# Kernel tuning notes

Measured on AMD Instinct MI355X. Metric: run time of the kernel, lower is better.

The kernel has to match this reference:

```python
import jax, jax.numpy as jnp
import numpy as np

B, T, W, L, H, TW = 2, 4096, 2048, 2048, 8, 4
HD = L // H  # head dim for block-diagonal gate projections


def setup_inputs() -> dict:
    key = jax.random.key(0)
    ks = jax.random.split(key, 16)
    inv_sqrt_w = 1.0 / np.sqrt(W)
    inv_sqrt_l = 1.0 / np.sqrt(L)
    inv_sqrt_hd = 1.0 / np.sqrt(HD)
    return {
        "x": jax.random.normal(ks[0], (B, T, W), dtype=jnp.float32),
        "segment_pos": jnp.tile(jnp.arange(T, dtype=jnp.int32), (B, 1)),
        # linear_y, linear_x: width -> lru_width
        "w_y": jax.random.normal(ks[1], (W, L), dtype=jnp.float32) * inv_sqrt_w,
        "b_y": jnp.zeros((L,), dtype=jnp.float32),
        "w_x": jax.random.normal(ks[2], (W, L), dtype=jnp.float32) * inv_sqrt_w,
        "b_x": jnp.zeros((L,), dtype=jnp.float32),
        # linear_out: lru_width -> width
        "w_out": jax.random.normal(ks[3], (L, W), dtype=jnp.float32) * inv_sqrt_l,
        "b_out": jnp.zeros((W,), dtype=jnp.float32),
        # depthwise causal temporal conv, kernel [TW, L]
        "conv_w": jax.random.normal(ks[4], (TW, L), dtype=jnp.float32) / np.sqrt(TW),
        "conv_b": jnp.zeros((L,), dtype=jnp.float32),
        # RG-LRU: a_param and two block-diagonal gate projections
        "a_param": jax.random.uniform(ks[5], (L,), dtype=jnp.float32, minval=-2.0, maxval=1.0),
        "igate_w": jax.random.normal(ks[6], (H, HD, HD), dtype=jnp.float32) * inv_sqrt_hd,
        "igate_b": jnp.zeros((H, HD), dtype=jnp.float32),
        "agate_w": jax.random.normal(ks[7], (H, HD, HD), dtype=jnp.float32) * inv_sqrt_hd,
        "agate_b": jnp.zeros((H, HD), dtype=jnp.float32),
    }


def _block_diag_linear(u, w, b):
    # u: [B,T,L] -> [B,T,H,HD] blockwise projected -> [B,T,L]
    uh = u.reshape(u.shape[0], u.shape[1], H, HD)
    y = jnp.einsum("bthd,hde->bthe", uh, w) + b
    return y.reshape(u.shape)


def _forward(x, segment_pos, w_y, b_y, w_x, b_x, w_out, b_out,
             conv_w, conv_b, a_param, igate_w, igate_b, agate_w, agate_b):
    # gate branch: linear_y + tanh-approx GELU
    y = jax.nn.gelu(jnp.einsum("btw,wl->btl", x, w_y) + b_y, approximate=True)
    # recurrent branch: linear_x
    xb = jnp.einsum("btw,wl->btl", x, w_x) + b_x
    # causal depthwise temporal conv (width TW), zero history before t=0
    x_pad = jnp.pad(xb, ((0, 0), (TW - 1, 0), (0, 0)))
    conv = conv_b + sum(conv_w[j] * x_pad[:, j:j + T] for j in range(TW))
    # RG-LRU gates
    gate_x = jax.nn.sigmoid(_block_diag_linear(conv, igate_w, igate_b))
    gate_a = jax.nn.sigmoid(_block_diag_linear(conv, agate_w, agate_b))
    log_a = -8.0 * gate_a * jax.nn.softplus(a_param)  # [B,T,L]
    a = jnp.exp(log_a)
    reset = (segment_pos == 0)[..., None]  # [B,T,1]
    multiplier = jnp.sqrt(1.0 - jnp.exp(2.0 * log_a))
    multiplier = jnp.where(reset, 1.0, multiplier)
    normed = conv * gate_x * multiplier
    a_masked = jnp.where(reset, 0.0, a)
    # diagonal linear recurrence: h_t = a_t * h_{t-1} + normed_t
    def step(h, inp):
        a_t, x_t = inp
        h = a_t * h + x_t
        return h, h
    h0 = jnp.zeros((x.shape[0], L), dtype=x.dtype)
    _, hs = jax.lax.scan(step, h0, (a_masked.transpose(1, 0, 2), normed.transpose(1, 0, 2)))
    hs = hs.transpose(1, 0, 2)  # [B,T,L]
    # elementwise gate then output projection
    return jnp.einsum("btl,lw->btw", hs * y, w_out) + b_out


def reference(x, segment_pos, w_y, b_y, w_x, b_x, w_out, b_out,
              conv_w, conv_b, a_param, igate_w, igate_b, agate_w, agate_b):
    return _forward(x, segment_pos, w_y, b_y, w_x, b_x, w_out, b_out,
                    conv_w, conv_b, a_param, igate_w, igate_b, agate_w, agate_b)
```

## Files before the change

kernel.cpp:

```cpp
#include <hip/hip_runtime.h>
#include <cstdint>
#include <math.h>

typedef _Float16 f16;
typedef f16 f16x8 __attribute__((ext_vector_type(8)));
typedef f16 f16x4 __attribute__((ext_vector_type(4)));
typedef float f32x4 __attribute__((ext_vector_type(4)));

#define BATCH 2
#define TSEQ 4096
#define WID 2048
#define LRU 2048
#define NHEAD 8
#define HDIM 256
#define MTOT (BATCH * TSEQ)
#define CT 128
#define NC (TSEQ / CT)

__device__ __forceinline__ void gl2lds16(const f16* g, f16* l) {
  __builtin_amdgcn_global_load_lds(
      (__attribute__((address_space(1))) uint32_t*)(uintptr_t)g,
      (__attribute__((address_space(3))) uint32_t*)(uint32_t)(uintptr_t)l,
      16, 0, 0);
}

__device__ __forceinline__ float sigmoidf_(float x) { return 1.f / (1.f + expf(-x)); }
__device__ __forceinline__ float f16bits_to_f(uint32_t b) {
  return (float)__builtin_bit_cast(f16, (uint16_t)b);
}

__global__ void prep_kernel(const float* __restrict__ x, f16* __restrict__ Xh,
                            const float* __restrict__ w_y, const float* __restrict__ w_x,
                            const float* __restrict__ w_out,
                            f16* __restrict__ wyT, f16* __restrict__ wxT, f16* __restrict__ woutT,
                            const float* __restrict__ ig, const float* __restrict__ ag,
                            f16* __restrict__ igT, f16* __restrict__ agT) {
  __shared__ float tile[32][33];
  const int bid = blockIdx.x, t = threadIdx.x;
  if (bid < 16384) {
    int i = bid * 256 + t;
    float4 v = ((const float4*)x)[i];
    f16x4 o = { (f16)v.x, (f16)v.y, (f16)v.z, (f16)v.w };
    ((f16x4*)Xh)[i] = o;
    return;
  }
  const int tx = t & 31, ty = t >> 5;
  const float* ib; f16* ob; int R, C, c0, r0;
  if (bid < 28672) {
    int idx = bid - 16384;
    int z = idx >> 12, tl = idx & 4095;
    ib = z == 0 ? w_y : (z == 1 ? w_x : w_out);
    ob = z == 0 ? wyT : (z == 1 ? wxT : woutT);
    R = 2048; C = 2048;
    c0 = (tl & 63) * 32; r0 = (tl >> 6) * 32;
  } else {
    int idx = bid - 28672;
    int z = idx >> 6, tl = idx & 63;
    ib = (z < 8 ? ig : ag) + (long long)(z & 7) * HDIM * HDIM;
    ob = (z < 8 ? igT : agT) + (long long)(z & 7) * HDIM * HDIM;
    R = HDIM; C = HDIM;
    c0 = (tl & 7) * 32; r0 = (tl >> 3) * 32;
  }
#pragma unroll
  for (int i = 0; i < 32; i += 8)
    tile[ty + i][tx] = ib[(long long)(r0 + ty + i) * C + c0 + tx];
  __syncthreads();
#pragma unroll
  for (int i = 0; i < 32; i += 8)
    ob[(long long)(c0 + ty + i) * R + r0 + tx] = (f16)tile[tx][ty + i];
}

__global__ __launch_bounds__(256, 2) void gemm_dual(
    const f16* __restrict__ A, const f16* __restrict__ B1T, const f16* __restrict__ B2T,
    const float* __restrict__ b1, const float* __restrict__ b2,
    f16* __restrict__ Y, f16* __restrict__ X2, int M, int N, int K) {
  __shared__ __align__(16) f16 As[128 * 32];
  __shared__ __align__(16) f16 B1s[128 * 32];
  __shared__ __align__(16) f16 B2s[128 * 32];
  const int m0 = blockIdx.x * 128, n0 = blockIdx.y * 128;
  const int t = threadIdx.x;
  const int lane = t & 63, wave = t >> 6;
  const int wr = (wave >> 1) * 64, wc = (wave & 1) * 64;
  const int l15 = lane & 15, quad = lane >> 4;
  const int srow = t >> 2, scol = (t & 3) * 8;

  const f16* Ag = A + (long long)(m0 + srow) * K + scol;
  const f16* B1g = B1T + (long long)(n0 + srow) * K + scol;
  const f16* B2g = B2T + (long long)(n0 + srow) * K + scol;

  f32x4 c1[4][4] = {};
  f32x4 c2[4][4] = {};
  for (int k0 = 0; k0 < K; k0 += 32) {
    gl2lds16(Ag, &As[t * 8]);   gl2lds16(Ag + (long long)64 * K, &As[64 * 32 + t * 8]);
    gl2lds16(B1g, &B1s[t * 8]); gl2lds16(B1g + (long long)64 * K, &B1s[64 * 32 + t * 8]);
    gl2lds16(B2g, &B2s[t * 8]); gl2lds16(B2g + (long long)64 * K, &B2s[64 * 32 + t * 8]);
    Ag += 32; B1g += 32; B2g += 32;
    __syncthreads();
    f16x8 af[4], b1f[4], b2f[4];
#pragma unroll
    for (int i = 0; i < 4; ++i)
      af[i] = *(const f16x8*)&As[(wr + i * 16 + l15) * 32 + quad * 8];
#pragma unroll
    for (int j = 0; j < 4; ++j) {
      b1f[j] = *(const f16x8*)&B1s[(wc + j * 16 + l15) * 32 + quad * 8];
      b2f[j] = *(const f16x8*)&B2s[(wc + j * 16 + l15) * 32 + quad * 8];
    }
#pragma unroll
    for (int i = 0; i < 4; ++i)
#pragma unroll
      for (int j = 0; j < 4; ++j) {
        c1[i][j] = __builtin_amdgcn_mfma_f32_16x16x32_f16(af[i], b1f[j], c1[i][j], 0, 0, 0);
        c2[i][j] = __builtin_amdgcn_mfma_f32_16x16x32_f16(af[i], b2f[j], c2[i][j], 0, 0, 0);
      }
    __syncthreads();
  }
#pragma unroll
  for (int i = 0; i < 4; ++i) {
#pragma unroll
    for (int j = 0; j < 4; ++j) {
      const int col = n0 + wc + j * 16 + l15;
      const float b1v = b1[col], b2v = b2[col];
      const int row0 = m0 + wr + i * 16 + quad * 4;
#pragma unroll
      for (int r = 0; r < 4; ++r) {
        long long off = (long long)(row0 + r) * N + col;
        float v = c1[i][j][r] + b1v;
        float u = v + 0.044715f * v * v * v;
        float g = 0.5f * v * (1.f + tanhf(0.7978845608028654f * u));
        Y[off] = (f16)g;
        X2[off] = (f16)(c2[i][j][r] + b2v);
      }
    }
  }
}

__global__ __launch_bounds__(256, 2) void gemm_bt(
    const f16* __restrict__ A, const f16* __restrict__ BT, const float* __restrict__ bias,
    float* __restrict__ Cf, int M, int N, int K) {
  __shared__ __align__(16) f16 As[128 * 32];
  __shared__ __align__(16) f16 Bs[128 * 32];
  const int m0 = blockIdx.x * 128, n0 = blockIdx.y * 128;
  const int t = threadIdx.x;
  const int lane = t & 63, wave = t >> 6;
  const int wr = (wave >> 1) * 64, wc = (wave & 1) * 64;
  const int l15 = lane & 15, quad = lane >> 4;
  const int srow = t >> 2, scol = (t & 3) * 8;

  const f16* Ag = A + (long long)(m0 + srow) * K + scol;
  const f16* Bg = BT + (long long)(n0 + srow) * K + scol;

  f32x4 acc[4][4] = {};
  for (int k0 = 0; k0 < K; k0 += 32) {
    gl2lds16(Ag, &As[t * 8]); gl2lds16(Ag + (long long)64 * K, &As[64 * 32 + t * 8]);
    gl2lds16(Bg, &Bs[t * 8]); gl2lds16(Bg + (long long)64 * K, &Bs[64 * 32 + t * 8]);
    Ag += 32; Bg += 32;
    __syncthreads();
    f16x8 af[4], bf[4];
#pragma unroll
    for (int i = 0; i < 4; ++i)
      af[i] = *(const f16x8*)&As[(wr + i * 16 + l15) * 32 + quad * 8];
#pragma unroll
    for (int j = 0; j < 4; ++j)
      bf[j] = *(const f16x8*)&Bs[(wc + j * 16 + l15) * 32 + quad * 8];
#pragma unroll
    for (int i = 0; i < 4; ++i)
#pragma unroll
      for (int j = 0; j < 4; ++j)
        acc[i][j] = __builtin_amdgcn_mfma_f32_16x16x32_f16(af[i], bf[j], acc[i][j], 0, 0, 0);
    __syncthreads();
  }
#pragma unroll
  for (int i = 0; i < 4; ++i) {
#pragma unroll
    for (int j = 0; j < 4; ++j) {
      const int col = n0 + wc + j * 16 + l15;
      const float bv = bias[col];
      const int row0 = m0 + wr + i * 16 + quad * 4;
#pragma unroll
      for (int r = 0; r < 4; ++r)
        Cf[(long long)(row0 + r) * N + col] = acc[i][j][r] + bv;
    }
  }
}

__global__ __launch_bounds__(256, 2) void gates_fused(
    const f16* __restrict__ XBh, const float* __restrict__ cw, const float* __restrict__ cb,
    const f16* __restrict__ BiT, const f16* __restrict__ BaT,
    const float* __restrict__ ib, const float* __restrict__ ab,
    const float* __restrict__ a_param, const int* __restrict__ segpos,
    uint32_t* __restrict__ AN, float* __restrict__ Ac, float* __restrict__ Hc) {
  __shared__ __align__(16) f16 As[128 * 256];
  __shared__ __align__(16) f16 Bi[128 * 32];
  __shared__ __align__(16) f16 Ba[128 * 32];
  const int m0 = blockIdx.x * 128;
  const int h = blockIdx.y >> 1;
  const int half = blockIdx.y & 1;
  const int ncol0 = h * HDIM + half * 128;
  const int t = threadIdx.x;
  const int lane = t & 63, wave = t >> 6;
  const int wr = (wave >> 1) * 64, wc = (wave & 1) * 64;
  const int l15 = lane & 15, quad = lane >> 4;

#pragma unroll 4
  for (int it = 0; it < 16; ++it) {
    int idx = it * 256 + t;
    int r = idx >> 5, kc = idx & 31;
    int m = m0 + r, tpos = m & (TSEQ - 1);
    int colbase = h * HDIM + kc * 8;
    float acc[8];
    {
      float4 c0 = *(const float4*)&cb[colbase];
      float4 c1 = *(const float4*)&cb[colbase + 4];
      acc[0] = c0.x; acc[1] = c0.y; acc[2] = c0.z; acc[3] = c0.w;
      acc[4] = c1.x; acc[5] = c1.y; acc[6] = c1.z; acc[7] = c1.w;
    }
#pragma unroll
    for (int d = 0; d < 4; ++d) {
      if (tpos >= d) {
        f16x8 xv = *(const f16x8*)&XBh[(long long)(m - d) * LRU + colbase];
        float4 w0 = *(const float4*)&cw[(3 - d) * LRU + colbase];
        float4 w1 = *(const float4*)&cw[(3 - d) * LRU + colbase + 4];
        acc[0] += w0.x * (float)xv[0]; acc[1] += w0.y * (float)xv[1];
        acc[2] += w0.z * (float)xv[2]; acc[3] += w0.w * (float)xv[3];
        acc[4] += w1.x * (float)xv[4]; acc[5] += w1.y * (float)xv[5];
        acc[6] += w1.z * (float)xv[6]; acc[7] += w1.w * (float)xv[7];
      }
    }
    f16x8 o;
#pragma unroll
    for (int k = 0; k < 8; ++k) o[k] = (f16)acc[k];
    int gs = (kc & ~7) | ((kc ^ r) & 7);
    *(f16x8*)&As[r * 256 + gs * 8] = o;
  }
  __syncthreads();

  const int srow = t >> 2, scol = (t & 3) * 8;
  const f16* Big = BiT + (long long)(ncol0 + srow) * HDIM + scol;
  const f16* Bag = BaT + (long long)(ncol0 + srow) * HDIM + scol;
  f32x4 ci[4][4] = {};
  f32x4 ca[4][4] = {};
  for (int k0 = 0; k0 < HDIM; k0 += 32) {
    gl2lds16(Big, &Bi[t * 8]); gl2lds16(Big + 64 * HDIM, &Bi[64 * 32 + t * 8]);
    gl2lds16(Bag, &Ba[t * 8]); gl2lds16(Bag + 64 * HDIM, &Ba[64 * 32 + t * 8]);
    Big += 32; Bag += 32;
    __syncthreads();
    f16x8 af[4], bif[4], baf[4];
#pragma unroll
    for (int i = 0; i < 4; ++i) {
      int row = wr + i * 16 + l15;
      int g = (k0 >> 3) + quad;
      int gsw = (g & ~7) | ((g ^ row) & 7);
      af[i] = *(const f16x8*)&As[row * 256 + gsw * 8];
    }
#pragma unroll
    for (int j = 0; j < 4; ++j) {
      bif[j] = *(const f16x8*)&Bi[(wc + j * 16 + l15) * 32 + quad * 8];
      baf[j] = *(const f16x8*)&Ba[(wc + j * 16 + l15) * 32 + quad * 8];
    }
#pragma unroll
    for (int i = 0; i < 4; ++i)
#pragma unroll
      for (int j = 0; j < 4; ++j) {
        ci[i][j] = __builtin_amdgcn_mfma_f32_16x16x32_f16(af[i], bif[j], ci[i][j], 0, 0, 0);
        ca[i][j] = __builtin_amdgcn_mfma_f32_16x16x32_f16(af[i], baf[j], ca[i][j], 0, 0, 0);
      }
    __syncthreads();
  }

  const int mb = m0 >> 12;
  const int cch = (m0 & (TSEQ - 1)) >> 7;
  float Aw[4], hw[4];
#pragma unroll
  for (int j = 0; j < 4; ++j) {
    const int cl = wc + j * 16 + l15;
    const int col = ncol0 + cl;
    const float ibv = ib[col], abv = ab[col];
    const float sp = log1pf(expf(a_param[col]));
    float A4[4], h4[4];
#pragma unroll
    for (int i = 0; i < 4; ++i) {
      float Aseg = 1.f, hseg = 0.f;
#pragma unroll
      for (int r = 0; r < 4; ++r) {
        const int rowL = wr + i * 16 + quad * 4 + r;
        const int row = m0 + rowL;
        float gx = sigmoidf_(ci[i][j][r] + ibv);
        float ga = sigmoidf_(ca[i][j][r] + abv);
        float la = -8.f * ga * sp;
        bool rs = (segpos[row] == 0);
        float a = rs ? 0.f : expf(la);
        uint32_t afx = __float2uint_rn(a * 65536.f);
        if (afx > 65535u) afx = 65535u;
        float aq = (float)afx * (1.f / 65536.f);
        int cfull = half * 128 + cl;
        int g = cfull >> 3, e = cfull & 7;
        int gsw = (g & ~7) | ((g ^ rowL) & 7);
        float cv = (float)As[rowL * 256 + gsw * 8 + e];
        float mult = rs ? 1.f : sqrtf(fmaxf(1.f - aq * aq, 0.f));
        f16 nh = (f16)(cv * gx * mult);
        AN[(long long)row * LRU + col] =
            afx | ((uint32_t)__builtin_bit_cast(uint16_t, nh) << 16);
        float xq = (float)nh;
        hseg = aq * hseg + xq;
        Aseg *= aq;
      }
      A4[i] = Aseg; h4[i] = hseg;
    }
#pragma unroll
    for (int i = 0; i < 4; ++i) {
      float A = A4[i], hv = h4[i];
#pragma unroll
      for (int d = 1; d <= 2; d <<= 1) {
        int src = quad >= d ? lane - 16 * d : lane;
        float Ap = __shfl(A, src);
        float hp = __shfl(hv, src);
        if (quad >= d) { hv = A * hp + hv; A = Ap * A; }
      }
      A4[i] = __shfl(A, 48 + l15);
      h4[i] = __shfl(hv, 48 + l15);
    }
    float Awv = 1.f, hwv = 0.f;
#pragma unroll
    for (int i = 0; i < 4; ++i) { hwv = A4[i] * hwv + h4[i]; Awv *= A4[i]; }
    Aw[j] = Awv; hw[j] = hwv;
  }
  float* carry = (float*)Bi;
  __syncthreads();
  if (wr == 0 && quad == 0) {
#pragma unroll
    for (int j = 0; j < 4; ++j) {
      int cl = wc + j * 16 + l15;
      carry[cl * 2] = Aw[j]; carry[cl * 2 + 1] = hw[j];
    }
  }
  __syncthreads();
  if (wr == 64 && quad == 0) {
#pragma unroll
    for (int j = 0; j < 4; ++j) {
      int cl = wc + j * 16 + l15;
      float At = carry[cl * 2], ht = carry[cl * 2 + 1];
      float A = At * Aw[j];
      float hv = Aw[j] * ht + hw[j];
      int o = (mb * NC + cch) * LRU + ncol0 + cl;
      Ac[o] = A; Hc[o] = hv;
    }
  }
}

__global__ void scan23_kernel(const uint32_t* __restrict__ AN,
                              const float* __restrict__ Ac, const float* __restrict__ Hc,
                              const f16* __restrict__ Yh, f16* __restrict__ G) {
  int l = blockIdx.x * 256 + threadIdx.x;
  int c = blockIdx.y, b = blockIdx.z;
  float hv = 0.f;
  for (int cc = 0; cc < c; ++cc) {
    int o = (b * NC + cc) * LRU + l;
    hv = Ac[o] * hv + Hc[o];
  }
  long long base = ((long long)b * TSEQ + (long long)c * CT) * LRU + l;
#pragma unroll 4
  for (int s = 0; s < CT; ++s) {
    long long o = base + (long long)s * LRU;
    uint32_t p = AN[o];
    float a = (float)(p & 0xFFFFu) * (1.f / 65536.f);
    float x = f16bits_to_f(p >> 16);
    hv = a * hv + x;
    G[o] = (f16)(hv * (float)Yh[o]);
  }
}

extern "C" void kernel_launch(void* const* d_in, const int* in_sizes, int n_in,
                              void* d_out, int out_size, void* d_ws, size_t ws_size,
                              hipStream_t stream) {
  (void)in_sizes; (void)n_in; (void)out_size; (void)ws_size;
  const float* x          = (const float*)d_in[0];
  const int*   segment_pos= (const int*)d_in[1];
  const float* w_y        = (const float*)d_in[2];
  const float* b_y        = (const float*)d_in[3];
  const float* w_x        = (const float*)d_in[4];
  const float* b_x        = (const float*)d_in[5];
  const float* w_out      = (const float*)d_in[6];
  const float* b_out      = (const float*)d_in[7];
  const float* conv_w     = (const float*)d_in[8];
  const float* conv_b     = (const float*)d_in[9];
  const float* a_param    = (const float*)d_in[10];
  const float* igate_w    = (const float*)d_in[11];
  const float* igate_b    = (const float*)d_in[12];
  const float* agate_w    = (const float*)d_in[13];
  const float* agate_b    = (const float*)d_in[14];
  float* out = (float*)d_out;

  char* base = (char*)d_ws;
  size_t off = 0;
  auto alloc = [&](size_t nbytes) -> void* {
    void* p = base + off;
    off = (off + nbytes + 255) & ~(size_t)255;
    return p;
  };
  f16*     Xh    = (f16*)alloc((size_t)MTOT * LRU * 2);
  f16*     Yh    = (f16*)alloc((size_t)MTOT * LRU * 2);
  f16*     XBh   = (f16*)alloc((size_t)MTOT * LRU * 2);
  uint32_t* AN   = (uint32_t*)alloc((size_t)MTOT * LRU * 4);
  f16*     wyT   = (f16*)alloc((size_t)WID * LRU * 2);
  f16*     wxT   = (f16*)alloc((size_t)WID * LRU * 2);
  f16*     woutT = (f16*)alloc((size_t)LRU * WID * 2);
  f16*     igwT  = (f16*)alloc((size_t)NHEAD * HDIM * HDIM * 2);
  f16*     agwT  = (f16*)alloc((size_t)NHEAD * HDIM * HDIM * 2);
  float*   Ac    = (float*)alloc((size_t)BATCH * NC * LRU * 4);
  float*   Hc    = (float*)alloc((size_t)BATCH * NC * LRU * 4);
  f16*     G     = Xh;

  prep_kernel<<<29696, 256, 0, stream>>>(x, Xh, w_y, w_x, w_out, wyT, wxT, woutT,
                                         igate_w, agate_w, igwT, agwT);
  gemm_dual<<<dim3(MTOT / 128, LRU / 128), 256, 0, stream>>>(
      Xh, wyT, wxT, b_y, b_x, Yh, XBh, MTOT, LRU, WID);
  gates_fused<<<dim3(MTOT / 128, 2 * NHEAD), 256, 0, stream>>>(
      XBh, conv_w, conv_b, igwT, agwT, igate_b, agate_b, a_param, segment_pos, AN, Ac, Hc);
  scan23_kernel<<<dim3(LRU / 256, NC, BATCH), 256, 0, stream>>>(AN, Ac, Hc, Yh, G);
  gemm_bt<<<dim3(MTOT / 128, WID / 128), 256, 0, stream>>>(G, woutT, b_out, out, MTOT, WID, LRU);
}
```

Baseline: 555.4 us.

## Triple-buffer LDS in both GEMMs with async prefetch and XOR swizzle

Both the dual-projection GEMM and the output GEMM now keep three LDS stages and prefetch two K-tiles ahead using direct global-to-LDS loads. Explicit vmcnt waits replace the double __syncthreads per iteration, so global loads overlap MFMA work. An XOR swizzle on the LDS column is meant to reduce bank conflicts on fragment reads, and s_setprio raises wave priority around the MFMA block. The cost is triple the LDS footprint (72KB for gemm_dual), which may limit occupancy below the two blocks per CU the launch bounds request. Correctness also now depends on hand-counted vmcnt values.

```diff
diff --git a/kernel.cpp b/kernel.cpp
--- a/kernel.cpp
+++ b/kernel.cpp
@@ -74,37 +74,52 @@
     const f16* __restrict__ A, const f16* __restrict__ B1T, const f16* __restrict__ B2T,
     const float* __restrict__ b1, const float* __restrict__ b2,
     f16* __restrict__ Y, f16* __restrict__ X2, int M, int N, int K) {
-  __shared__ __align__(16) f16 As[128 * 32];
-  __shared__ __align__(16) f16 B1s[128 * 32];
-  __shared__ __align__(16) f16 B2s[128 * 32];
+  __shared__ __align__(16) f16 As[3][128 * 32];
+  __shared__ __align__(16) f16 B1s[3][128 * 32];
+  __shared__ __align__(16) f16 B2s[3][128 * 32];
   const int m0 = blockIdx.x * 128, n0 = blockIdx.y * 128;
   const int t = threadIdx.x;
   const int lane = t & 63, wave = t >> 6;
   const int wr = (wave >> 1) * 64, wc = (wave & 1) * 64;
   const int l15 = lane & 15, quad = lane >> 4;
-  const int srow = t >> 2, scol = (t & 3) * 8;
+  const int srow = t >> 2;
+  const int scol = ((t & 3) ^ ((srow >> 1) & 3)) * 8;
+  const int sl = (quad ^ ((l15 >> 1) & 3)) * 8;
 
   const f16* Ag = A + (long long)(m0 + srow) * K + scol;
   const f16* B1g = B1T + (long long)(n0 + srow) * K + scol;
   const f16* B2g = B2T + (long long)(n0 + srow) * K + scol;
+  const long long h64 = (long long)64 * K;
+
+  auto STAGE = [&](int tt, int bb) {
+    const f16* a = Ag + tt * 32;
+    const f16* p1 = B1g + tt * 32;
+    const f16* p2 = B2g + tt * 32;
+    gl2lds16(a, &As[bb][t * 8]);    gl2lds16(a + h64, &As[bb][64 * 32 + t * 8]);
+    gl2lds16(p1, &B1s[bb][t * 8]);  gl2lds16(p1 + h64, &B1s[bb][64 * 32 + t * 8]);
+    gl2lds16(p2, &B2s[bb][t * 8]);  gl2lds16(p2 + h64, &B2s[bb][64 * 32 + t * 8]);
+  };
 
   f32x4 c1[4][4] = {};
   f32x4 c2[4][4] = {};
-  for (int k0 = 0; k0 < K; k0 += 32) {
-    gl2lds16(Ag, &As[t * 8]);   gl2lds16(Ag + (long long)64 * K, &As[64 * 32 + t * 8]);
-    gl2lds16(B1g, &B1s[t * 8]); gl2lds16(B1g + (long long)64 * K, &B1s[64 * 32 + t * 8]);
-    gl2lds16(B2g, &B2s[t * 8]); gl2lds16(B2g + (long long)64 * K, &B2s[64 * 32 + t * 8]);
-    Ag += 32; B1g += 32; B2g += 32;
-    __syncthreads();
+  const int NT = K >> 5;
+  STAGE(0, 0); STAGE(1, 1);
+  asm volatile("s_waitcnt vmcnt(6)" ::: "memory");
+  __builtin_amdgcn_s_barrier();
+  __builtin_amdgcn_sched_barrier(0);
+  int bufc = 0, bufs = 2;
+  for (int tt = 0; tt < NT; ++tt) {
+    if (tt + 2 < NT) STAGE(tt + 2, bufs);
     f16x8 af[4], b1f[4], b2f[4];
 #pragma unroll
     for (int i = 0; i < 4; ++i)
-      af[i] = *(const f16x8*)&As[(wr + i * 16 + l15) * 32 + quad * 8];
-#pragma unroll
-    for (int j = 0; j < 4; ++j) {
-      b1f[j] = *(const f16x8*)&B1s[(wc + j * 16 + l15) * 32 + quad * 8];
-      b2f[j] = *(const f16x8*)&B2s[(wc + j * 16 + l15) * 32 + quad * 8];
-    }
+      af[i] = *(const f16x8*)&As[bufc][(wr + i * 16 + l15) * 32 + sl];
+#pragma unroll
+    for (int j = 0; j < 4; ++j) {
+      b1f[j] = *(const f16x8*)&B1s[bufc][(wc + j * 16 + l15) * 32 + sl];
+      b2f[j] = *(const f16x8*)&B2s[bufc][(wc + j * 16 + l15) * 32 + sl];
+    }
+    __builtin_amdgcn_s_setprio(1);
 #pragma unroll
     for (int i = 0; i < 4; ++i)
 #pragma unroll
@@ -112,7 +127,15 @@
         c1[i][j] = __builtin_amdgcn_mfma_f32_16x16x32_f16(af[i], b1f[j], c1[i][j], 0, 0, 0);
         c2[i][j] = __builtin_amdgcn_mfma_f32_16x16x32_f16(af[i], b2f[j], c2[i][j], 0, 0, 0);
       }
-    __syncthreads();
+    __builtin_amdgcn_s_setprio(0);
+    if (tt + 1 < NT) {
+      if (tt + 2 < NT) { asm volatile("s_waitcnt vmcnt(6)" ::: "memory"); }
+      else             { asm volatile("s_waitcnt vmcnt(0)" ::: "memory"); }
+      __builtin_amdgcn_s_barrier();
+      __builtin_amdgcn_sched_barrier(0);
+    }
+    bufc = (bufc + 1 == 3) ? 0 : bufc + 1;
+    bufs = (bufs + 1 == 3) ? 0 : bufs + 1;
   }
 #pragma unroll
   for (int i = 0; i < 4; ++i) {
@@ -137,37 +160,59 @@
 __global__ __launch_bounds__(256, 2) void gemm_bt(
     const f16* __restrict__ A, const f16* __restrict__ BT, const float* __restrict__ bias,
     float* __restrict__ Cf, int M, int N, int K) {
-  __shared__ __align__(16) f16 As[128 * 32];
-  __shared__ __align__(16) f16 Bs[128 * 32];
+  __shared__ __align__(16) f16 As[3][128 * 32];
+  __shared__ __align__(16) f16 Bs[3][128 * 32];
   const int m0 = blockIdx.x * 128, n0 = blockIdx.y * 128;
   const int t = threadIdx.x;
   const int lane = t & 63, wave = t >> 6;
   const int wr = (wave >> 1) * 64, wc = (wave & 1) * 64;
   const int l15 = lane & 15, quad = lane >> 4;
-  const int srow = t >> 2, scol = (t & 3) * 8;
+  const int srow = t >> 2;
+  const int scol = ((t & 3) ^ ((srow >> 1) & 3)) * 8;
+  const int sl = (quad ^ ((l15 >> 1) & 3)) * 8;
 
   const f16* Ag = A + (long long)(m0 + srow) * K + scol;
   const f16* Bg = BT + (long long)(n0 + srow) * K + scol;
+  const long long h64 = (long long)64 * K;
+
+  auto STAGE = [&](int tt, int bb) {
+    const f16* a = Ag + tt * 32;
+    const f16* p = Bg + tt * 32;
+    gl2lds16(a, &As[bb][t * 8]); gl2lds16(a + h64, &As[bb][64 * 32 + t * 8]);
+    gl2lds16(p, &Bs[bb][t * 8]); gl2lds16(p + h64, &Bs[bb][64 * 32 + t * 8]);
+  };
 
   f32x4 acc[4][4] = {};
-  for (int k0 = 0; k0 < K; k0 += 32) {
-    gl2lds16(Ag, &As[t * 8]); gl2lds16(Ag + (long long)64 * K, &As[64 * 32 + t * 8]);
-    gl2lds16(Bg, &Bs[t * 8]); gl2lds16(Bg + (long long)64 * K, &Bs[64 * 32 + t * 8]);
-    Ag += 32; Bg += 32;
-    __syncthreads();
+  const int NT = K >> 5;
+  STAGE(0, 0); STAGE(1, 1);
+  asm volatile("s_waitcnt vmcnt(4)" ::: "memory");
+  __builtin_amdgcn_s_barrier();
+  __builtin_amdgcn_sched_barrier(0);
+  int bufc = 0, bufs = 2;
+  for (int tt = 0; tt < NT; ++tt) {
+    if (tt + 2 < NT) STAGE(tt + 2, bufs);
     f16x8 af[4], bf[4];
 #pragma unroll
     for (int i = 0; i < 4; ++i)
-      af[i] = *(const f16x8*)&As[(wr + i * 16 + l15) * 32 + quad * 8];
+      af[i] = *(const f16x8*)&As[bufc][(wr + i * 16 + l15) * 32 + sl];
 #pragma unroll
     for (int j = 0; j < 4; ++j)
-      bf[j] = *(const f16x8*)&Bs[(wc + j * 16 + l15) * 32 + quad * 8];
+      bf[j] = *(const f16x8*)&Bs[bufc][(wc + j * 16 + l15) * 32 + sl];
+    __builtin_amdgcn_s_setprio(1);
 #pragma unroll
     for (int i = 0; i < 4; ++i)
 #pragma unroll
       for (int j = 0; j < 4; ++j)
         acc[i][j] = __builtin_amdgcn_mfma_f32_16x16x32_f16(af[i], bf[j], acc[i][j], 0, 0, 0);
-    __syncthreads();
+    __builtin_amdgcn_s_setprio(0);
+    if (tt + 1 < NT) {
+      if (tt + 2 < NT) { asm volatile("s_waitcnt vmcnt(4)" ::: "memory"); }
+      else             { asm volatile("s_waitcnt vmcnt(0)" ::: "memory"); }
+      __builtin_amdgcn_s_barrier();
+      __builtin_amdgcn_sched_barrier(0);
+    }
+    bufc = (bufc + 1 == 3) ? 0 : bufc + 1;
+    bufs = (bufs + 1 == 3) ? 0 : bufs + 1;
   }
 #pragma unroll
   for (int i = 0; i < 4; ++i) {
```

Result: no change. 558.2 us (+0.5%).
